# Performance work log

Measured on AMD Instinct MI355X. Metric: run time of the kernel, lower is better.

## Reference

```python
import jax, jax.numpy as jnp
import numpy as np

N = 1024
NEVAL = 131072
NUM_POLES = 8
DOMAIN = (-1.0, 1.0)
DOMAIN_LEN = DOMAIN[1] - DOMAIN[0]
EPS = 1e-14


def _cheb_nodes(n):
    # Chebyshev points of the second kind: cos(pi * linspace(0, 1, n))
    return jnp.cos(jnp.pi * jnp.linspace(0.0, 1.0, n))


def _to_standard(x):
    return 2.0 * (x - DOMAIN[0]) / DOMAIN_LEN - 1.0


def _barycentric_weights(nodes, poles_real, poles_imag):
    # Vectorized equivalent of the original per-node Python loop.
    n = nodes.shape[0]
    diff = nodes[:, None] - nodes[None, :]            # (N, N)
    eye = jnp.eye(n, dtype=bool)
    # log_weights[j] = -sum_{i!=j} log|nodes[j]-nodes[i]|
    log_w = -jnp.sum(jnp.log(jnp.where(eye, 1.0, jnp.abs(diff))), axis=1)
    # signs[j] = (-1)^(# of negative off-diagonal diffs); diagonal diff==0 contributes nothing
    neg_count = jnp.sum(diff < 0, axis=1)
    signs = jnp.where(neg_count % 2 == 0, 1.0, -1.0)
    # each conjugate pole pair contributes 2*log(sqrt((x-r)^2 + i^2)) = log((x-r)^2 + i^2)
    pole_term = jnp.log((nodes[:, None] - poles_real[None, :]) ** 2
                        + poles_imag[None, :] ** 2)   # (N, M)
    log_w = log_w + jnp.sum(pole_term, axis=1)
    log_w = log_w - jnp.max(log_w)
    w = signs * jnp.exp(log_w)
    return w / jnp.abs(w[0])


def setup_inputs() -> dict:
    key = jax.random.key(0)
    k1, k2, k3, k4 = jax.random.split(key, 4)
    x_eval = jax.random.uniform(k1, (NEVAL,), dtype=jnp.float32)  # in [0,1) subset of domain
    values = jax.random.normal(k2, (N,), dtype=jnp.float32)
    poles_real = jax.random.normal(k3, (NUM_POLES,), dtype=jnp.float32)
    poles_imag = jax.random.normal(k4, (NUM_POLES,), dtype=jnp.float32)
    return {"x_eval": x_eval, "values": values,
            "poles_real": poles_real, "poles_imag": poles_imag}


def reference(x_eval, values, poles_real, poles_imag):
    nodes = _cheb_nodes(N)
    nodes_std = _to_standard(nodes)                   # identity for domain (-1,1)
    w = _barycentric_weights(nodes, poles_real, poles_imag)

    x_std = _to_standard(x_eval)
    d_x = x_std[None, :] - nodes_std[:, None]         # (N, NEVAL)
    small = jnp.abs(d_x) < EPS
    small_any = jnp.any(small, axis=0)                # (NEVAL,)
    d_safe = jnp.where(small, 1.0, d_x)
    inv = jnp.where(small_any[None, :], 0.0, 1.0 / d_safe)
    inv = jnp.where(small, 1.0, inv)                  # exact-hit columns: indicator row -> 1

    num = jnp.einsum('n,nm,n->m', values, inv, w)
    den = jnp.einsum('nm,n->m', inv, w)
    return num / den
```

## Files before the change

### kernel.cpp

```cpp
#include <hip/hip_runtime.h>
#include <math.h>

#define N_NODES 1024
#define N_EVAL 131072
#define NUM_POLES 8
#define PI_D 3.14159265358979323846

__global__ void wk_setup(const float* __restrict__ values,
                         const float* __restrict__ poles_real,
                         const float* __restrict__ poles_imag,
                         float4* __restrict__ pk) {
    const int j = blockIdx.x * 128 + threadIdx.x;
    const double nd = cos(PI_D * (double)j / (double)(N_NODES - 1));
    double prod = (j == 0 || j == N_NODES - 1) ? 0.5 : 1.0;
#pragma unroll
    for (int m = 0; m < NUM_POLES; ++m) {
        const double dr = nd - (double)poles_real[m];
        const double di = (double)poles_imag[m];
        prod *= dr * dr + di * di;
    }
    if (j & 1) prod = -prod;
    pk[j] = make_float4((float)nd, (float)prod,
                        (float)(prod * (double)values[j]), 0.0f);
}

__global__ __launch_bounds__(512) void eval_kernel(
    const float* __restrict__ x_eval,
    const float4* __restrict__ pk,
    float* __restrict__ out) {
    __shared__ __align__(16) float s_n[N_NODES];
    __shared__ __align__(16) float s_w[N_NODES];
    __shared__ __align__(16) float s_v[N_NODES];
    __shared__ float2 s_r[8][128];

    const int t = threadIdx.x;

#pragma unroll
    for (int h = 0; h < 2; ++h) {
        const int j = t + h * 512;
        const float4 e = pk[j];
        s_n[j] = e.x;
        s_w[j] = e.y;
        s_v[j] = e.z;
    }
    __syncthreads();

    const int lane = t & 63;
    const int wid  = t >> 6;
    const int pbase = blockIdx.x * 128;
    const float x0 = x_eval[pbase + lane];
    const float x1 = x_eval[pbase + 64 + lane];

    const float4* n4 = (const float4*)s_n + wid * 32;
    const float4* w4 = (const float4*)s_w + wid * 32;
    const float4* v4 = (const float4*)s_v + wid * 32;

    float a0 = 0.0f, b0 = 0.0f;
    float a1 = 0.0f, b1 = 0.0f;

#define NODE(C)                                                            \
    {                                                                      \
        const float d0 = x0 - an.C;                                        \
        const float d1 = x1 - an.C;                                        \
        const float r0 = __builtin_amdgcn_rcpf(d0);                        \
        const float r1 = __builtin_amdgcn_rcpf(d1);                        \
        a0 = fmaf(av.C, r0, a0); b0 = fmaf(aw.C, r0, b0);                  \
        a1 = fmaf(av.C, r1, a1); b1 = fmaf(aw.C, r1, b1);                  \
    }

#pragma unroll 4
    for (int q = 0; q < 32; ++q) {
        const float4 an = n4[q];
        const float4 aw = w4[q];
        const float4 av = v4[q];
        NODE(x) NODE(y) NODE(z) NODE(w)
    }
#undef NODE

    s_r[wid][lane]      = make_float2(a0, b0);
    s_r[wid][lane + 64] = make_float2(a1, b1);
    __syncthreads();

    if (t < 128) {
        float nn = 0.0f, dd = 0.0f;
#pragma unroll
        for (int w = 0; w < 8; ++w) {
            const float2 pr = s_r[w][t];
            nn += pr.x;
            dd += pr.y;
        }
        float res = nn / dd;
        if (__builtin_expect(__builtin_isnan(res), 0)) {
            const float x = x_eval[pbase + t];
            float hn = 0.0f, hd = 0.0f;
            for (int j = 0; j < N_NODES; ++j) {
                const float4 e = pk[j];
                if (e.x == x) { hn += e.z; hd += e.y; }
            }
            res = hn / hd;
        }
        out[pbase + t] = res;
    }
}

extern "C" void kernel_launch(void* const* d_in, const int* in_sizes, int n_in,
                              void* d_out, int out_size, void* d_ws, size_t ws_size,
                              hipStream_t stream) {
    const float* x_eval     = (const float*)d_in[0];
    const float* values     = (const float*)d_in[1];
    const float* poles_real = (const float*)d_in[2];
    const float* poles_imag = (const float*)d_in[3];
    float* out = (float*)d_out;

    float4* pk = (float4*)d_ws;

    wk_setup<<<8, 128, 0, stream>>>(values, poles_real, poles_imag, pk);
    eval_kernel<<<N_EVAL / 128, 512, 0, stream>>>(x_eval, pk, out);
}
```

Before: 133.5 us.

## Pair nodes to share one reciprocal and enlarge blocks to 1024 threads

Processes two nodes per step: one hardware reciprocal of the product (x-nA)(x-nB) is multiplied by each difference to get both 1/(x-nA) and 1/(x-nB), halving the number of rcp transcendental ops. Blocks grow to 1024 threads covering 256 evaluation points, with 16 waves each handling 64 nodes and four points per thread. This trades rcp throughput for extra multiplies and more register pressure, and adds overflow/underflow risk in the product. The fallback path now also catches inf results.

Result: no change. 131.7 us (-1.3%).

```diff
diff --git a/kernel.cpp b/kernel.cpp
--- a/kernel.cpp
+++ b/kernel.cpp
@@ -24,73 +24,90 @@
                         (float)(prod * (double)values[j]), 0.0f);
 }
 
-__global__ __launch_bounds__(512) void eval_kernel(
+__global__ __launch_bounds__(1024, 8) void eval_kernel(
     const float* __restrict__ x_eval,
     const float4* __restrict__ pk,
     float* __restrict__ out) {
     __shared__ __align__(16) float s_n[N_NODES];
     __shared__ __align__(16) float s_w[N_NODES];
     __shared__ __align__(16) float s_v[N_NODES];
-    __shared__ float2 s_r[8][128];
+    __shared__ float2 s_r[16][256];
 
     const int t = threadIdx.x;
 
-#pragma unroll
-    for (int h = 0; h < 2; ++h) {
-        const int j = t + h * 512;
-        const float4 e = pk[j];
-        s_n[j] = e.x;
-        s_w[j] = e.y;
-        s_v[j] = e.z;
+    {
+        const float4 e = pk[t];
+        s_n[t] = e.x;
+        s_w[t] = e.y;
+        s_v[t] = e.z;
     }
     __syncthreads();
 
     const int lane = t & 63;
     const int wid  = t >> 6;
-    const int pbase = blockIdx.x * 128;
+    const int pbase = blockIdx.x * 256;
     const float x0 = x_eval[pbase + lane];
     const float x1 = x_eval[pbase + 64 + lane];
+    const float x2 = x_eval[pbase + 128 + lane];
+    const float x3 = x_eval[pbase + 192 + lane];
 
-    const float4* n4 = (const float4*)s_n + wid * 32;
-    const float4* w4 = (const float4*)s_w + wid * 32;
-    const float4* v4 = (const float4*)s_v + wid * 32;
+    const float4* n4 = (const float4*)s_n + wid * 16;
+    const float4* w4 = (const float4*)s_w + wid * 16;
+    const float4* v4 = (const float4*)s_v + wid * 16;
 
-    float a0 = 0.0f, b0 = 0.0f;
-    float a1 = 0.0f, b1 = 0.0f;
+    float a0 = 0.0f, b0 = 0.0f, a1 = 0.0f, b1 = 0.0f;
+    float a2 = 0.0f, b2 = 0.0f, a3 = 0.0f, b3 = 0.0f;
 
-#define NODE(C)                                                            \
+#define PAIR(nA, wA, vA, nB, wB, vB)                                       \
     {                                                                      \
-        const float d0 = x0 - an.C;                                        \
-        const float d1 = x1 - an.C;                                        \
-        const float r0 = __builtin_amdgcn_rcpf(d0);                        \
-        const float r1 = __builtin_amdgcn_rcpf(d1);                        \
-        a0 = fmaf(av.C, r0, a0); b0 = fmaf(aw.C, r0, b0);                  \
-        a1 = fmaf(av.C, r1, a1); b1 = fmaf(aw.C, r1, b1);                  \
+        const float dA0 = x0 - (nA), dB0 = x1 - (nA);                      \
+        const float dA1 = x2 - (nA), dB1 = x3 - (nA);                      \
+        const float eA0 = x0 - (nB), eB0 = x1 - (nB);                      \
+        const float eA1 = x2 - (nB), eB1 = x3 - (nB);                      \
+        const float r0 = __builtin_amdgcn_rcpf(dA0 * eA0);                 \
+        const float r1 = __builtin_amdgcn_rcpf(dB0 * eB0);                 \
+        const float r2 = __builtin_amdgcn_rcpf(dA1 * eA1);                 \
+        const float r3 = __builtin_amdgcn_rcpf(dB1 * eB1);                 \
+        const float iA0 = r0 * eA0, iB0 = r0 * dA0;                        \
+        const float iA1 = r1 * eB0, iB1 = r1 * dB0;                        \
+        const float iA2 = r2 * eA1, iB2 = r2 * dA1;                        \
+        const float iA3 = r3 * eB1, iB3 = r3 * dB1;                        \
+        a0 = fmaf((vA), iA0, a0); b0 = fmaf((wA), iA0, b0);                \
+        a0 = fmaf((vB), iB0, a0); b0 = fmaf((wB), iB0, b0);                \
+        a1 = fmaf((vA), iA1, a1); b1 = fmaf((wA), iA1, b1);                \
+        a1 = fmaf((vB), iB1, a1); b1 = fmaf((wB), iB1, b1);                \
+        a2 = fmaf((vA), iA2, a2); b2 = fmaf((wA), iA2, b2);                \
+        a2 = fmaf((vB), iB2, a2); b2 = fmaf((wB), iB2, b2);                \
+        a3 = fmaf((vA), iA3, a3); b3 = fmaf((wA), iA3, b3);                \
+        a3 = fmaf((vB), iB3, a3); b3 = fmaf((wB), iB3, b3);                \
     }
 
-#pragma unroll 4
-    for (int q = 0; q < 32; ++q) {
+#pragma unroll 2
+    for (int q = 0; q < 16; ++q) {
         const float4 an = n4[q];
         const float4 aw = w4[q];
         const float4 av = v4[q];
-        NODE(x) NODE(y) NODE(z) NODE(w)
+        PAIR(an.x, aw.x, av.x, an.y, aw.y, av.y)
+        PAIR(an.z, aw.z, av.z, an.w, aw.w, av.w)
     }
-#undef NODE
+#undef PAIR
 
-    s_r[wid][lane]      = make_float2(a0, b0);
-    s_r[wid][lane + 64] = make_float2(a1, b1);
+    s_r[wid][lane]       = make_float2(a0, b0);
+    s_r[wid][lane + 64]  = make_float2(a1, b1);
+    s_r[wid][lane + 128] = make_float2(a2, b2);
+    s_r[wid][lane + 192] = make_float2(a3, b3);
     __syncthreads();
 
-    if (t < 128) {
+    if (t < 256) {
         float nn = 0.0f, dd = 0.0f;
 #pragma unroll
-        for (int w = 0; w < 8; ++w) {
+        for (int w = 0; w < 16; ++w) {
             const float2 pr = s_r[w][t];
             nn += pr.x;
             dd += pr.y;
         }
         float res = nn / dd;
-        if (__builtin_expect(__builtin_isnan(res), 0)) {
+        if (__builtin_expect(__builtin_isnan(res) | __builtin_isinf(res), 0)) {
             const float x = x_eval[pbase + t];
             float hn = 0.0f, hd = 0.0f;
             for (int j = 0; j < N_NODES; ++j) {
@@ -115,5 +132,5 @@
     float4* pk = (float4*)d_ws;
 
     wk_setup<<<8, 128, 0, stream>>>(values, poles_real, poles_imag, pk);
-    eval_kernel<<<N_EVAL / 128, 512, 0, stream>>>(x_eval, pk, out);
+    eval_kernel<<<N_EVAL / 256, 1024, 0, stream>>>(x_eval, pk, out);
 }
```
